# Performance work log

Measured on AMD Instinct MI355X. Metric: run time of the kernel, lower is better.

The kernel has to match this reference:

```python
import jax, jax.numpy as jnp
import numpy as np

N_HEAD = 8
T_THRESHOLD = 0.001


def setup_inputs() -> dict:
    key = jax.random.key(0)
    ks = jax.random.split(key, 5)
    B, N, NL, R = 4, 1024, 4, 256
    C = NL * R
    x = jax.random.normal(ks[0], (B, N, NL, R), dtype=jnp.float32)
    Wc = jax.random.normal(ks[1], (R, 3 * R), dtype=jnp.float32) * (1.0 / np.sqrt(R))
    bc = jnp.zeros((3 * R,), dtype=jnp.float32)
    Wp = jax.random.normal(ks[2], (C, C), dtype=jnp.float32) * (1.0 / np.sqrt(C))
    bp = jnp.zeros((C,), dtype=jnp.float32)
    return {"x": x, "Wc": Wc, "bc": bc, "Wp": Wp, "bp": bp}


def reference(x, Wc, bc, Wp, bp):
    B, N, NL, R = x.shape
    H = N_HEAD
    D = R // H  # head dim
    # shared per-level qkv projection: (B, N, NL, 3R)
    qkv = x @ Wc + bc
    q, k, v = jnp.split(qkv, 3, axis=-1)
    # split heads: (B, N, NL, H, D)
    q = q.reshape(B, N, NL, H, D)
    k = k.reshape(B, N, NL, H, D)
    v = v.reshape(B, N, NL, H, D)
    scale = 1.0 / np.sqrt(D).astype(np.float32)
    # per-level attention scores: (B, NL, H, N, N)
    att = jnp.einsum('bnlhd,bmlhd->blhnm', q, k) * scale
    att = jax.nn.softmax(att, axis=-1)
    # custom post-softmax thresholding (ReLU(softmax - T)); dropout is identity at eval
    att = jax.nn.relu(att - T_THRESHOLD)
    # multiply attentions across levels: low parent attention dooms the child
    comb = jnp.prod(att, axis=1)  # (B, H, N, N)
    # apply combined attention to each level's values: (B, N, NL, H, D)
    y = jnp.einsum('bhnm,bmlhd->bnlhd', comb, v)
    y = y.reshape(B, N, NL * H * D)  # (B, N, C)
    y = y @ Wp + bp  # c_proj; resid dropout identity at eval
    return y.reshape(B, N, NL, R)
```

## Files before the change

### kernel.cpp

```cpp
#include <hip/hip_runtime.h>

#define TTHR 0.001f
#define QSC2 0.25503486f
#define CAP 16
#define YSCALE 8388608.0f
#define YINV   1.1920928955078125e-07f

#if __has_builtin(__builtin_amdgcn_exp2f)
#define EXP2(x) __builtin_amdgcn_exp2f(x)
#else
#define EXP2(x) __expf((x) * 0.6931471805599453f)
#endif

typedef _Float16 half4v __attribute__((ext_vector_type(4)));
typedef _Float16 half8v __attribute__((ext_vector_type(8)));
typedef float f32x4 __attribute__((ext_vector_type(4)));

__device__ __forceinline__ int xcd_bid() {
  return (blockIdx.x & 7) * ((int)gridDim.x >> 3) + ((int)blockIdx.x >> 3);
}

__device__ __forceinline__ void stage_tile_s(const _Float16* __restrict__ gsrc,
                                             int rowstride, _Float16* lds, int tid)
{
  const int lane = tid & 63;
  const int w4 = (tid >> 6) << 2;
#pragma unroll
  for (int r = 0; r < 4; ++r) {
    const int p = (w4 + r) * 64 + lane;
    const int row = p >> 3, xg = p & 7;
    __builtin_amdgcn_global_load_lds(
        (const __attribute__((address_space(1))) void*)(gsrc + row * rowstride + ((xg ^ (row & 7)) << 3)),
        (__attribute__((address_space(3))) void*)(lds + (w4 + r) * 512),
        16, 0, 0);
  }
}

__device__ __forceinline__ void stage_tile64(const _Float16* __restrict__ gsrc,
                                             int rowstride, _Float16* lds, int tid)
{
  const int lane = tid & 63;
  const int w2 = (tid >> 6) << 1;
#pragma unroll
  for (int r = 0; r < 2; ++r) {
    const int p = (w2 + r) * 64 + lane;
    const int row = p >> 3, xg = p & 7;
    __builtin_amdgcn_global_load_lds(
        (const __attribute__((address_space(1))) void*)(gsrc + row * rowstride + ((xg ^ (row & 7)) << 3)),
        (__attribute__((address_space(3))) void*)(lds + (w2 + r) * 512),
        16, 0, 0);
  }
}

__device__ __forceinline__ void stage_q64_512(const _Float16* __restrict__ gsrc,
                                              _Float16* lds, int tid)
{
  const int lane = tid & 63, w = tid >> 6;
  const int p = (w << 6) + lane;
  const int row = p >> 3, xg = p & 7;
  __builtin_amdgcn_global_load_lds(
      (const __attribute__((address_space(1))) void*)(gsrc + row * 64 + ((xg ^ (row & 7)) << 3)),
      (__attribute__((address_space(3))) void*)(lds + (w << 9)),
      16, 0, 0);
}

__device__ __forceinline__ void stage_k128_512(const _Float16* __restrict__ gsrc,
                                               _Float16* lds, int tid)
{
  const int lane = tid & 63, w = tid >> 6;
#pragma unroll
  for (int r = 0; r < 2; ++r) {
    const int p = ((w << 1) + r) * 64 + lane;
    const int row = p >> 3, xg = p & 7;
    __builtin_amdgcn_global_load_lds(
        (const __attribute__((address_space(1))) void*)(gsrc + row * 64 + ((xg ^ (row & 7)) << 3)),
        (__attribute__((address_space(3))) void*)(lds + ((w << 1) + r) * 512),
        16, 0, 0);
  }
}

__global__ __launch_bounds__(256) void k_split_rm(
    const float* __restrict__ in, _Float16* __restrict__ oh,
    _Float16* __restrict__ ol, int n4)
{
  const int i = blockIdx.x * 256 + threadIdx.x;
  if (i >= n4) return;
  float4 v = ((const float4*)in)[i];
  half4v h = {(_Float16)v.x, (_Float16)v.y, (_Float16)v.z, (_Float16)v.w};
  half4v l = {(_Float16)(v.x - (float)h[0]), (_Float16)(v.y - (float)h[1]),
              (_Float16)(v.z - (float)h[2]), (_Float16)(v.w - (float)h[3])};
  ((half4v*)oh)[i] = h;
  ((half4v*)ol)[i] = l;
}

__global__ __launch_bounds__(256) void k_split_tr(
    const float* __restrict__ in, _Float16* __restrict__ oh,
    _Float16* __restrict__ ol, int K, int N)
{
  __shared__ float t[32][33];
  const int nb = N >> 5;
  const int n0 = (blockIdx.x % nb) << 5, k0 = (blockIdx.x / nb) << 5;
  const int r = threadIdx.x >> 3, c4 = (threadIdx.x & 7) << 2;
  float4 v = *(const float4*)&in[(k0 + r) * N + n0 + c4];
  t[r][c4] = v.x; t[r][c4 + 1] = v.y; t[r][c4 + 2] = v.z; t[r][c4 + 3] = v.w;
  __syncthreads();
  float a0 = t[c4][r], a1 = t[c4 + 1][r], a2 = t[c4 + 2][r], a3 = t[c4 + 3][r];
  half4v h = {(_Float16)a0, (_Float16)a1, (_Float16)a2, (_Float16)a3};
  half4v l = {(_Float16)(a0 - (float)h[0]), (_Float16)(a1 - (float)h[1]),
              (_Float16)(a2 - (float)h[2]), (_Float16)(a3 - (float)h[3])};
  *(half4v*)&oh[(n0 + r) * K + k0 + c4] = h;
  *(half4v*)&ol[(n0 + r) * K + k0 + c4] = l;
}

template<int EPI>
__global__ __launch_bounds__(256) void k_gemm_split(
    const _Float16* __restrict__ Ah, const _Float16* __restrict__ Al,
    const _Float16* __restrict__ Bh, const _Float16* __restrict__ Bl,
    const float* __restrict__ bias, int K, int kclog, int nbn,
    float* __restrict__ out, _Float16* __restrict__ Qs,
    _Float16* __restrict__ Ks, float* __restrict__ Vp)
{
  __shared__ __align__(16) _Float16 Asm[3][8192];
  __shared__ __align__(16) _Float16 Bsm[3][4096];
  const int tid = threadIdx.x, lane = tid & 63, w = tid >> 6;
  const int wr = w >> 1, wc = w & 1;
  const int lrow = lane & 15, lk = lane >> 4;
  const int bid = xcd_bid();
  const int mt = bid / nbn, ct = bid % nbn;
  const int m0 = mt << 7, c0 = ct << 6;

  const int nch = 3 << kclog;
  const int kcm = (1 << kclog) - 1;

  auto abase = [&](int c2) -> const _Float16* {
    const int phase = c2 >> kclog, kc = c2 & kcm;
    const _Float16* A = (phase == 2) ? Al : Ah;
    return A + (size_t)m0 * K + (kc << 6);
  };
  auto bbase = [&](int c2) -> const _Float16* {
    const int phase = c2 >> kclog, kc = c2 & kcm;
    const _Float16* B = (phase == 1) ? Bl : Bh;
    return B + (size_t)c0 * K + (kc << 6);
  };

  stage_tile_s(abase(0), K, Asm[0], tid);
  stage_tile64(bbase(0), K, Bsm[0], tid);
  stage_tile_s(abase(1), K, Asm[1], tid);
  stage_tile64(bbase(1), K, Bsm[1], tid);

  f32x4 acc[4][2] = {};
  int cur = 0;
#pragma unroll 1
  for (int ch = 0; ch < nch; ++ch) {
    if (ch + 1 < nch) { asm volatile("s_waitcnt vmcnt(6)" ::: "memory"); }
    else              { asm volatile("s_waitcnt vmcnt(0)" ::: "memory"); }
    __builtin_amdgcn_s_barrier();
    __builtin_amdgcn_sched_barrier(0);
#pragma unroll
    for (int ks = 0; ks < 2; ++ks) {
      half8v af[4], bf[2];
#pragma unroll
      for (int mi = 0; mi < 4; ++mi) {
        const int row = (wr << 6) + (mi << 4) + lrow;
        const int xg = ((ks << 2) + lk) ^ (row & 7);
        af[mi] = *(const half8v*)&Asm[cur][((row << 3) + xg) << 3];
      }
#pragma unroll
      for (int ni = 0; ni < 2; ++ni) {
        const int col = (wc << 5) + (ni << 4) + lrow;
        const int xg = ((ks << 2) + lk) ^ (col & 7);
        bf[ni] = *(const half8v*)&Bsm[cur][((col << 3) + xg) << 3];
      }
#pragma unroll
      for (int mi = 0; mi < 4; ++mi)
#pragma unroll
        for (int ni = 0; ni < 2; ++ni)
          acc[mi][ni] = __builtin_amdgcn_mfma_f32_16x16x32_f16(af[mi], bf[ni], acc[mi][ni], 0, 0, 0);
    }
    if (ch + 2 < nch) {
      int nb = cur + 2; if (nb >= 3) nb -= 3;
      stage_tile_s(abase(ch + 2), K, Asm[nb], tid);
      stage_tile64(bbase(ch + 2), K, Bsm[nb], tid);
    }
    ++cur; if (cur == 3) cur = 0;
  }

#pragma unroll
  for (int ni = 0; ni < 2; ++ni) {
    const int c = c0 + (wc << 5) + (ni << 4) + lrow;
    const float bv = bias[c];
    if (EPI == 0) {
#pragma unroll
      for (int mi = 0; mi < 4; ++mi)
#pragma unroll
        for (int reg = 0; reg < 4; ++reg) {
          const int m = m0 + (wr << 6) + (mi << 4) + (lk << 2) + reg;
          out[m * 1024 + c] = acc[mi][ni][reg] * YINV + bv;
        }
    } else {
      const int part = c >> 8, cc = c & 255;
      const int h = cc >> 5, d = cc & 31;
#pragma unroll
      for (int mi = 0; mi < 4; ++mi)
#pragma unroll
        for (int reg = 0; reg < 4; ++reg) {
          const int m = m0 + (wr << 6) + (mi << 4) + (lk << 2) + reg;
          const int b = m >> 12, n = (m >> 2) & 1023, l = m & 3;
          const int panel = b * 32 + l * 8 + h;
          float v = acc[mi][ni][reg] + bv;
          if (part == 2) {
            Vp[(panel << 15) + n * 32 + d] = v;
          } else {
            _Float16* dst = part ? Ks : Qs;
            if (!part) v *= QSC2;
            _Float16 hv = (_Float16)v;
            _Float16 lv = (_Float16)(v - (float)hv);
            dst[(panel << 16) + n * 64 + d] = hv;
            dst[(panel << 16) + n * 64 + 32 + d] = lv;
          }
        }
    }
  }
}

__global__ __launch_bounds__(512) void k_att(
    const _Float16* __restrict__ Qs, const _Float16* __restrict__ Ks,
    int* __restrict__ ccnt, unsigned short* __restrict__ cidx,
    float* __restrict__ cval)
{
  __shared__ __align__(16) _Float16 Qres[4][4096];
  __shared__ __align__(16) _Float16 Kb[2][8192];
  __shared__ float Zsh[4][64];
  __shared__ float tzs[4][64];
  __shared__ float rz[64];
  __shared__ int lcnt[64];
  const int tid = threadIdx.x, lane = tid & 63, w = tid >> 6;
  const int wr = w >> 2, wc = w & 3;
  const int lrow = lane & 15, lk = lane >> 4;
  const int s = (blockIdx.x & 7) * 64 + ((int)blockIdx.x >> 3);
  const int bh = s >> 4, rt = s & 15;
  const int b = bh >> 3, h = bh & 7;
  const int pbase = b * 32 + h;

#pragma unroll
  for (int l = 0; l < 4; ++l)
    stage_q64_512(Qs + ((pbase + l * 8) << 16) + (rt << 12), Qres[l], tid);
  stage_k128_512(Ks + (pbase << 16), Kb[0], tid);
  if (tid < 256) Zsh[tid >> 6][tid & 63] = 0.0f;
  __syncthreads();

  const int kstB[2] = {0, 4};
  float rsum[2][4] = {};
  float prod[2][2][4];

#pragma unroll 1
  for (int it = 0; it < 64; ++it) {
    const int cur = it & 1;
    const int pass = it >> 5;
    const int l  = pass ? ((it - 32) & 3) : (it >> 3);
    const int ct = pass ? ((it - 32) >> 2) : (it & 7);
    if (it < 63) {
      const int t2 = it + 1;
      const int l2  = (t2 < 32) ? (t2 >> 3) : ((t2 - 32) & 3);
      const int ct2 = (t2 < 32) ? (t2 & 7) : ((t2 - 32) >> 2);
      stage_k128_512(Ks + ((pbase + l2 * 8) << 16) + (ct2 << 13), Kb[cur ^ 1], tid);
    }
    if (pass && l == 0 && tid < 64) lcnt[tid] = 0;

    f32x4 acc[2][2] = {};
#pragma unroll
    for (int ks = 0; ks < 2; ++ks) {
      half8v af[2], bf[2];
#pragma unroll
      for (int mi = 0; mi < 2; ++mi) {
        const int row = (wr << 5) + (mi << 4) + lrow;
        const int xg = lk ^ (row & 7);
        af[mi] = *(const half8v*)&Qres[l][((row << 3) + xg) << 3];
      }
#pragma unroll
      for (int ni = 0; ni < 2; ++ni) {
        const int col = (wc << 5) + (ni << 4) + lrow;
        const int xg = (kstB[ks] + lk) ^ (col & 7);
        bf[ni] = *(const half8v*)&Kb[cur][((col << 3) + xg) << 3];
      }
#pragma unroll
      for (int mi = 0; mi < 2; ++mi)
#pragma unroll
        for (int ni = 0; ni < 2; ++ni)
          acc[mi][ni] = __builtin_amdgcn_mfma_f32_16x16x32_f16(af[mi], bf[ni], acc[mi][ni], 0, 0, 0);
    }

    if (!pass) {
#pragma unroll
      for (int mi = 0; mi < 2; ++mi)
#pragma unroll
        for (int reg = 0; reg < 4; ++reg)
          rsum[mi][reg] += EXP2(acc[mi][0][reg]) + EXP2(acc[mi][1][reg]);
      if ((it & 7) == 7) {
#pragma unroll
        for (int mi = 0; mi < 2; ++mi)
#pragma unroll
          for (int reg = 0; reg < 4; ++reg) {
            float v = rsum[mi][reg];
            v += __shfl_xor(v, 1, 64);
            v += __shfl_xor(v, 2, 64);
            v += __shfl_xor(v, 4, 64);
            v += __shfl_xor(v, 8, 64);
            if (lrow == 0)
              atomicAdd(&Zsh[l][(wr << 5) + (mi << 4) + (lk << 2) + reg], v);
            rsum[mi][reg] = 0.0f;
          }
      }
    } else {
#pragma unroll
      for (int mi = 0; mi < 2; ++mi)
#pragma unroll
        for (int reg = 0; reg < 4; ++reg) {
          const float tzv = tzs[l][(wr << 5) + (mi << 4) + (lk << 2) + reg];
#pragma unroll
          for (int ni = 0; ni < 2; ++ni) {
            const float e = fmaxf(EXP2(acc[mi][ni][reg]) - tzv, 0.0f);
            prod[mi][ni][reg] = (l == 0) ? e : prod[mi][ni][reg] * e;
          }
        }
      if (l == 3) {
#pragma unroll
        for (int mi = 0; mi < 2; ++mi)
#pragma unroll
          for (int ni = 0; ni < 2; ++ni)
#pragma unroll
            for (int reg = 0; reg < 4; ++reg) {
              const int rloc = (wr << 5) + (mi << 4) + (lk << 2) + reg;
              const float v = prod[mi][ni][reg] * rz[rloc];
              if (v > 0.0f) {
                const int slot = atomicAdd(&lcnt[rloc], 1);
                if (slot < CAP) {
                  const int rowc = (bh << 10) + (rt << 6) + rloc;
                  const int mglob = (ct << 7) + (wc << 5) + (ni << 4) + lrow;
                  cidx[(rowc * 8 + ct) * CAP + slot] = (unsigned short)mglob;
                  cval[(rowc * 8 + ct) * CAP + slot] = v * YSCALE;
                }
              }
            }
        __syncthreads();
        if (tid < 64)
          ccnt[((bh << 10) + (rt << 6) + tid) * 8 + ct] = min(lcnt[tid], CAP);
      }
    }
    __syncthreads();
    if (it == 31) {
      if (tid < 256) tzs[tid >> 6][tid & 63] = TTHR * Zsh[tid >> 6][tid & 63];
      if (tid < 64)
        rz[tid] = 1.0f / ((Zsh[0][tid] * Zsh[1][tid]) * (Zsh[2][tid] * Zsh[3][tid]));
      __syncthreads();
    }
  }
}

__global__ __launch_bounds__(512) void k_pv(
    const float* __restrict__ Vp, const int* __restrict__ ccnt,
    const unsigned short* __restrict__ cidx, const float* __restrict__ cval,
    _Float16* __restrict__ ysh, _Float16* __restrict__ ysl)
{
  const int rowc = blockIdx.x * 8 + (threadIdx.x >> 6);
  const int lane = threadIdx.x & 63;
  const int bh = rowc >> 10, n = rowc & 1023;
  const int b = bh >> 3, h = bh & 7;
  const int l0 = lane >> 5, d = lane & 31;
  const float* vA = Vp + ((b * 32 + l0 * 8 + h) << 15) + d;
  const float* vB = vA + (16 << 15);
  float y0 = 0.f, y1 = 0.f;
  for (int mcj = 0; mcj < 8; ++mcj) {
    const int cnt = min(ccnt[rowc * 8 + mcj], CAP);
    const int off = (rowc * 8 + mcj) * CAP;
    for (int i = 0; i < cnt; ++i) {
      const int m = cidx[off + i];
      const float wv = cval[off + i];
      y0 = fmaf(wv, vA[m * 32], y0);
      y1 = fmaf(wv, vB[m * 32], y1);
    }
  }
  const int idx = ((b << 10) + n) * 1024 + l0 * 256 + h * 32 + d;
  _Float16 h0 = (_Float16)y0;
  ysh[idx] = h0;
  ysl[idx] = (_Float16)(y0 - (float)h0);
  _Float16 h1 = (_Float16)y1;
  ysh[idx + 512] = h1;
  ysl[idx + 512] = (_Float16)(y1 - (float)h1);
}

extern "C" void kernel_launch(void* const* d_in, const int* in_sizes, int n_in,
                              void* d_out, int out_size, void* d_ws, size_t ws_size,
                              hipStream_t stream)
{
  const float* x  = (const float*)d_in[0];
  const float* Wc = (const float*)d_in[1];
  const float* bc = (const float*)d_in[2];
  const float* Wp = (const float*)d_in[3];
  const float* bp = (const float*)d_in[4];
  float* out = (float*)d_out;
  (void)in_sizes; (void)n_in; (void)out_size;

  if (ws_size < 98828288ull) return;
  char* wsb = (char*)d_ws;
  float*          Vp   = (float*)wsb;
  _Float16*       Qs   = (_Float16*)(wsb + 16777216);
  _Float16*       Ks   = (_Float16*)(wsb + 33554432);
  _Float16*       xh   = (_Float16*)(wsb + 50855936);
  _Float16*       xl   = (_Float16*)(wsb + 59244544);
  int*            ccnt = (int*)(wsb + 67633152);
  unsigned short* cidx = (unsigned short*)(wsb + 68681728);
  float*          cval = (float*)(wsb + 77070336);
  _Float16*       Wch  = (_Float16*)(wsb + 93847552);
  _Float16*       Wcl  = (_Float16*)(wsb + 94240768);
  _Float16*       Wph  = (_Float16*)(wsb + 94633984);
  _Float16*       Wpl  = (_Float16*)(wsb + 96731136);

  k_split_rm<<<dim3(4096), dim3(256), 0, stream>>>(x, xh, xl, 1048576);
  k_split_tr<<<dim3(192), dim3(256), 0, stream>>>(Wc, Wch, Wcl, 256, 768);
  k_split_tr<<<dim3(1024), dim3(256), 0, stream>>>(Wp, Wph, Wpl, 1024, 1024);
  k_gemm_split<1><<<dim3(1536), dim3(256), 0, stream>>>(
      xh, xl, Wch, Wcl, bc, 256, 2, 12, nullptr, Qs, Ks, Vp);
  k_att<<<dim3(512), dim3(512), 0, stream>>>(Qs, Ks, ccnt, cidx, cval);
  k_pv<<<dim3(4096), dim3(512), 0, stream>>>(Vp, ccnt, cidx, cval, xh, xl);
  k_gemm_split<0><<<dim3(512), dim3(256), 0, stream>>>(
      xh, xl, Wph, Wpl, bp, 1024, 4, 16, out, nullptr, nullptr, nullptr);
}
```

Before: 223.2 us.

## Double attention-score block to 1024 threads with narrower per-wave column tiles

The score kernel now launches 1024 threads per block. Each wave computes a 32x16 slice of the tile instead of 32x32, which roughly halves per-wave MFMA, exp and compaction work and raises the number of resident waves. Only the high-half Q fragment is staged into shared memory, since the low half was never read, so the Q staging buffer shrinks and the per-wave staging helpers become inline lambdas. The launch bound with a minimum-occupancy hint may cap register use and cause spills. More waves also contend on the shared-memory atomics and barriers.

```diff
diff --git a/kernel.cpp b/kernel.cpp
--- a/kernel.cpp
+++ b/kernel.cpp
@@ -48,33 +48,6 @@
     __builtin_amdgcn_global_load_lds(
         (const __attribute__((address_space(1))) void*)(gsrc + row * rowstride + ((xg ^ (row & 7)) << 3)),
         (__attribute__((address_space(3))) void*)(lds + (w2 + r) * 512),
-        16, 0, 0);
-  }
-}
-
-__device__ __forceinline__ void stage_q64_512(const _Float16* __restrict__ gsrc,
-                                              _Float16* lds, int tid)
-{
-  const int lane = tid & 63, w = tid >> 6;
-  const int p = (w << 6) + lane;
-  const int row = p >> 3, xg = p & 7;
-  __builtin_amdgcn_global_load_lds(
-      (const __attribute__((address_space(1))) void*)(gsrc + row * 64 + ((xg ^ (row & 7)) << 3)),
-      (__attribute__((address_space(3))) void*)(lds + (w << 9)),
-      16, 0, 0);
-}
-
-__device__ __forceinline__ void stage_k128_512(const _Float16* __restrict__ gsrc,
-                                               _Float16* lds, int tid)
-{
-  const int lane = tid & 63, w = tid >> 6;
-#pragma unroll
-  for (int r = 0; r < 2; ++r) {
-    const int p = ((w << 1) + r) * 64 + lane;
-    const int row = p >> 3, xg = p & 7;
-    __builtin_amdgcn_global_load_lds(
-        (const __attribute__((address_space(1))) void*)(gsrc + row * 64 + ((xg ^ (row & 7)) << 3)),
-        (__attribute__((address_space(3))) void*)(lds + ((w << 1) + r) * 512),
         16, 0, 0);
   }
 }
@@ -223,35 +196,55 @@
   }
 }
 
-__global__ __launch_bounds__(512) void k_att(
+__global__ __launch_bounds__(1024, 8) void k_att(
     const _Float16* __restrict__ Qs, const _Float16* __restrict__ Ks,
     int* __restrict__ ccnt, unsigned short* __restrict__ cidx,
     float* __restrict__ cval)
 {
-  __shared__ __align__(16) _Float16 Qres[4][4096];
+  __shared__ __align__(16) _Float16 Qres[4][2048];
   __shared__ __align__(16) _Float16 Kb[2][8192];
   __shared__ float Zsh[4][64];
   __shared__ float tzs[4][64];
   __shared__ float rz[64];
   __shared__ int lcnt[64];
   const int tid = threadIdx.x, lane = tid & 63, w = tid >> 6;
-  const int wr = w >> 2, wc = w & 3;
+  const int wr = w >> 3, wc = w & 7;
   const int lrow = lane & 15, lk = lane >> 4;
   const int s = (blockIdx.x & 7) * 64 + ((int)blockIdx.x >> 3);
   const int bh = s >> 4, rt = s & 15;
   const int b = bh >> 3, h = bh & 7;
   const int pbase = b * 32 + h;
 
-#pragma unroll
-  for (int l = 0; l < 4; ++l)
-    stage_q64_512(Qs + ((pbase + l * 8) << 16) + (rt << 12), Qres[l], tid);
-  stage_k128_512(Ks + (pbase << 16), Kb[0], tid);
+  auto kaddr = [&](int t) -> const _Float16* {
+    const int l  = (t < 32) ? (t >> 3) : ((t - 32) & 3);
+    const int ct = (t < 32) ? (t & 7) : ((t - 32) >> 2);
+    return Ks + ((size_t)(pbase + l * 8) << 16) + (ct << 13);
+  };
+  auto stage_k = [&](const _Float16* kb2, _Float16* lds) {
+    const int row = tid >> 3, xg = tid & 7;
+    __builtin_amdgcn_global_load_lds(
+        (const __attribute__((address_space(1))) void*)(kb2 + row * 64 + ((xg ^ (row & 7)) << 3)),
+        (__attribute__((address_space(3))) void*)(lds + (w << 9)),
+        16, 0, 0);
+  };
+
+  {
+    const int l = w >> 2;
+    const int p = ((w & 3) << 6) + lane;
+    const int row = p >> 2, xg = p & 3;
+    __builtin_amdgcn_global_load_lds(
+        (const __attribute__((address_space(1))) void*)(
+            Qs + ((size_t)(pbase + l * 8) << 16) + (rt << 12)
+               + row * 64 + ((xg ^ (row & 3)) << 3)),
+        (__attribute__((address_space(3))) void*)(&Qres[l][(w & 3) << 9]),
+        16, 0, 0);
+  }
+  stage_k(kaddr(0), Kb[0]);
   if (tid < 256) Zsh[tid >> 6][tid & 63] = 0.0f;
   __syncthreads();
 
-  const int kstB[2] = {0, 4};
   float rsum[2][4] = {};
-  float prod[2][2][4];
+  float prod[2][4];
 
 #pragma unroll 1
   for (int it = 0; it < 64; ++it) {
@@ -259,35 +252,24 @@
     const int pass = it >> 5;
     const int l  = pass ? ((it - 32) & 3) : (it >> 3);
     const int ct = pass ? ((it - 32) >> 2) : (it & 7);
-    if (it < 63) {
-      const int t2 = it + 1;
-      const int l2  = (t2 < 32) ? (t2 >> 3) : ((t2 - 32) & 3);
-      const int ct2 = (t2 < 32) ? (t2 & 7) : ((t2 - 32) >> 2);
-      stage_k128_512(Ks + ((pbase + l2 * 8) << 16) + (ct2 << 13), Kb[cur ^ 1], tid);
-    }
+    if (it < 63) stage_k(kaddr(it + 1), Kb[cur ^ 1]);
     if (pass && l == 0 && tid < 64) lcnt[tid] = 0;
 
-    f32x4 acc[2][2] = {};
+    half8v af[2];
+#pragma unroll
+    for (int mi = 0; mi < 2; ++mi) {
+      const int row = (wr << 5) + (mi << 4) + lrow;
+      af[mi] = *(const half8v*)&Qres[l][(row << 5) + ((lk ^ (row & 3)) << 3)];
+    }
+    f32x4 acc[2] = {};
 #pragma unroll
     for (int ks = 0; ks < 2; ++ks) {
-      half8v af[2], bf[2];
-#pragma unroll
-      for (int mi = 0; mi < 2; ++mi) {
-        const int row = (wr << 5) + (mi << 4) + lrow;
-        const int xg = lk ^ (row & 7);
-        af[mi] = *(const half8v*)&Qres[l][((row << 3) + xg) << 3];
-      }
-#pragma unroll
-      for (int ni = 0; ni < 2; ++ni) {
-        const int col = (wc << 5) + (ni << 4) + lrow;
-        const int xg = (kstB[ks] + lk) ^ (col & 7);
-        bf[ni] = *(const half8v*)&Kb[cur][((col << 3) + xg) << 3];
-      }
+      const int col = (wc << 4) + lrow;
+      const int xg = ((ks << 2) + lk) ^ (col & 7);
+      half8v bf = *(const half8v*)&Kb[cur][((col << 3) + xg) << 3];
 #pragma unroll
       for (int mi = 0; mi < 2; ++mi)
-#pragma unroll
-        for (int ni = 0; ni < 2; ++ni)
-          acc[mi][ni] = __builtin_amdgcn_mfma_f32_16x16x32_f16(af[mi], bf[ni], acc[mi][ni], 0, 0, 0);
+        acc[mi] = __builtin_amdgcn_mfma_f32_16x16x32_f16(af[mi], bf, acc[mi], 0, 0, 0);
     }
 
     if (!pass) {
@@ -295,7 +277,7 @@
       for (int mi = 0; mi < 2; ++mi)
 #pragma unroll
         for (int reg = 0; reg < 4; ++reg)
-          rsum[mi][reg] += EXP2(acc[mi][0][reg]) + EXP2(acc[mi][1][reg]);
+          rsum[mi][reg] += EXP2(acc[mi][reg]);
       if ((it & 7) == 7) {
 #pragma unroll
         for (int mi = 0; mi < 2; ++mi)
@@ -317,31 +299,26 @@
 #pragma unroll
         for (int reg = 0; reg < 4; ++reg) {
           const float tzv = tzs[l][(wr << 5) + (mi << 4) + (lk << 2) + reg];
-#pragma unroll
-          for (int ni = 0; ni < 2; ++ni) {
-            const float e = fmaxf(EXP2(acc[mi][ni][reg]) - tzv, 0.0f);
-            prod[mi][ni][reg] = (l == 0) ? e : prod[mi][ni][reg] * e;
-          }
+          const float e = fmaxf(EXP2(acc[mi][reg]) - tzv, 0.0f);
+          prod[mi][reg] = (l == 0) ? e : prod[mi][reg] * e;
         }
       if (l == 3) {
 #pragma unroll
         for (int mi = 0; mi < 2; ++mi)
 #pragma unroll
-          for (int ni = 0; ni < 2; ++ni)
-#pragma unroll
-            for (int reg = 0; reg < 4; ++reg) {
-              const int rloc = (wr << 5) + (mi << 4) + (lk << 2) + reg;
-              const float v = prod[mi][ni][reg] * rz[rloc];
-              if (v > 0.0f) {
-                const int slot = atomicAdd(&lcnt[rloc], 1);
-                if (slot < CAP) {
-                  const int rowc = (bh << 10) + (rt << 6) + rloc;
-                  const int mglob = (ct << 7) + (wc << 5) + (ni << 4) + lrow;
-                  cidx[(rowc * 8 + ct) * CAP + slot] = (unsigned short)mglob;
-                  cval[(rowc * 8 + ct) * CAP + slot] = v * YSCALE;
-                }
+          for (int reg = 0; reg < 4; ++reg) {
+            const int rloc = (wr << 5) + (mi << 4) + (lk << 2) + reg;
+            const float v = prod[mi][reg] * rz[rloc];
+            if (v > 0.0f) {
+              const int slot = atomicAdd(&lcnt[rloc], 1);
+              if (slot < CAP) {
+                const int rowc = (bh << 10) + (rt << 6) + rloc;
+                const int mglob = (ct << 7) + (wc << 4) + lrow;
+                cidx[(rowc * 8 + ct) * CAP + slot] = (unsigned short)mglob;
+                cval[(rowc * 8 + ct) * CAP + slot] = v * YSCALE;
               }
             }
+          }
         __syncthreads();
         if (tid < 64)
           ccnt[((bh << 10) + (rt << 6) + tid) * 8 + ct] = min(lcnt[tid], CAP);
@@ -421,7 +398,7 @@
   k_split_tr<<<dim3(1024), dim3(256), 0, stream>>>(Wp, Wph, Wpl, 1024, 1024);
   k_gemm_split<1><<<dim3(1536), dim3(256), 0, stream>>>(
       xh, xl, Wch, Wcl, bc, 256, 2, 12, nullptr, Qs, Ks, Vp);
-  k_att<<<dim3(512), dim3(512), 0, stream>>>(Qs, Ks, ccnt, cidx, cval);
+  k_att<<<dim3(512), dim3(1024), 0, stream>>>(Qs, Ks, ccnt, cidx, cval);
   k_pv<<<dim3(4096), dim3(512), 0, stream>>>(Vp, ccnt, cidx, cval, xh, xl);
   k_gemm_split<0><<<dim3(512), dim3(256), 0, stream>>>(
       xh, xl, Wph, Wpl, bp, 1024, 4, 16, out, nullptr, nullptr, nullptr);
```

Result: slower. 235.8 us (+5.6%).
